# Optimization experiments

Hardware: AMD Instinct MI355X
Metric: run time of the kernel (lower is better)

## Reference

```python
import jax, jax.numpy as jnp
import numpy as np

BLOCK = 128
E, T, H, I, K = 16, 512, 2048, 1408, 6

def _dequant(w, s):
    # w: (E, R, C), s: (E, R//BLOCK, C//BLOCK) block-wise inverse scales
    return w * jnp.repeat(jnp.repeat(s, BLOCK, axis=1), BLOCK, axis=2)

def setup_inputs() -> dict:
    key = jax.random.key(0)
    ks = jax.random.split(key, 9)
    return {
        "x": jax.random.normal(ks[0], (T, H), dtype=jnp.float32),
        "gate_weights": jax.random.normal(ks[1], (E, I, H), dtype=jnp.float32) * 0.05,
        "gate_scales": jax.random.uniform(ks[2], (E, I // BLOCK, H // BLOCK), dtype=jnp.float32),
        "up_weights": jax.random.normal(ks[3], (E, I, H), dtype=jnp.float32) * 0.05,
        "up_scales": jax.random.uniform(ks[4], (E, I // BLOCK, H // BLOCK), dtype=jnp.float32),
        "down_weights": jax.random.normal(ks[5], (E, H, I), dtype=jnp.float32) * 0.05,
        "down_scales": jax.random.uniform(ks[6], (E, H // BLOCK, I // BLOCK), dtype=jnp.float32),
        "routing_weights": jax.random.uniform(ks[7], (T, K), dtype=jnp.float32),
        "selected_experts": jax.random.randint(ks[8], (T, K), 0, E, dtype=jnp.int32),
    }

def reference(x, gate_weights, gate_scales, up_weights, up_scales,
              down_weights, down_scales, routing_weights, selected_experts):
    # Dequantize block-quantized expert weights
    wg = _dequant(gate_weights, gate_scales)   # (E, I, H)
    wu = _dequant(up_weights, up_scales)       # (E, I, H)
    wd = _dequant(down_weights, down_scales)   # (E, H, I)
    # Dense per-expert grouped GEMMs (reference path: all experts see all tokens)
    g = jnp.einsum('th,eih->eti', x, wg)       # (E, T, I)
    u = jnp.einsum('th,eih->eti', x, wu)
    h = jax.nn.silu(g) * u                     # SwiGLU
    y = jnp.einsum('eti,ehi->eth', h, wd)      # (E, T, H)
    # Combine: top-k routing weights scattered to (T, E) then contracted
    onehot = jax.nn.one_hot(selected_experts, E, dtype=x.dtype)  # (T, K, E)
    combine = jnp.einsum('tk,tke->et', routing_weights, onehot)  # (E, T)
    return jnp.einsum('et,eth->th', combine, y)                  # (T, H)
```

## Files before the change

kernel.cpp:

```cpp
#include <hip/hip_runtime.h>
#include <stdint.h>

#define E_NUM 16
#define T_TOK 512
#define H_DIM 2048
#define I_DIM 1408
#define K_TOP 6
#define CAP   512

#define TM  256
#define TN  32
#define BK  64
#define LDA 72

typedef __attribute__((ext_vector_type(8))) __bf16 bf16x8;
typedef __attribute__((ext_vector_type(4))) float f32x4;
typedef __attribute__((ext_vector_type(4))) unsigned short us4;
typedef __attribute__((ext_vector_type(8))) unsigned short us8;

__device__ __forceinline__ unsigned short f2bf(float f) {
  union { float f; unsigned u; } v; v.f = f;
  unsigned r = v.u + 0x7FFFu + ((v.u >> 16) & 1u);
  return (unsigned short)(r >> 16);
}

__global__ void k_routing(const float* __restrict__ rw, const int* __restrict__ sel,
                          int* counts, int* list, float* cw) {
  int t = blockIdx.x * blockDim.x + threadIdx.x;
  if (t >= T_TOK) return;
  int e[K_TOP]; float w[K_TOP];
#pragma unroll
  for (int k = 0; k < K_TOP; ++k) { e[k] = sel[t*K_TOP+k]; w[k] = rw[t*K_TOP+k]; }
#pragma unroll
  for (int k = 0; k < K_TOP; ++k) {
    bool dup = false;
#pragma unroll
    for (int j = 0; j < K_TOP; ++j) if (j < k && e[j] == e[k]) dup = true;
    if (!dup) {
      float c = 0.f;
#pragma unroll
      for (int j = 0; j < K_TOP; ++j) if (e[j] == e[k]) c += w[j];
      int slot = atomicAdd(&counts[e[k]], 1);
      list[e[k]*CAP + slot] = t;
      cw[e[k]*CAP + slot] = c;
    }
  }
}

__global__ void k_xcast(const float* __restrict__ x, unsigned short* __restrict__ xb) {
  int i = blockIdx.x * blockDim.x + threadIdx.x;
  const float4* src = (const float4*)x;
  float4 v0 = src[2*i], v1 = src[2*i+1];
  us8 o;
  o[0]=f2bf(v0.x); o[1]=f2bf(v0.y); o[2]=f2bf(v0.z); o[3]=f2bf(v0.w);
  o[4]=f2bf(v1.x); o[5]=f2bf(v1.y); o[6]=f2bf(v1.z); o[7]=f2bf(v1.w);
  *(us8*)(xb + (size_t)i*8) = o;
}

__global__ __launch_bounds__(256, 2)
void k_gateup(const unsigned short* __restrict__ xb,
              const float* __restrict__ Wg, const float* __restrict__ Sg,
              const float* __restrict__ Wu, const float* __restrict__ Su,
              const int* __restrict__ counts, const int* __restrict__ list,
              const float* __restrict__ cw, unsigned short* __restrict__ Hbuf) {
  __shared__ unsigned short sA[TM * LDA];
  __shared__ unsigned short sB[2 * TN * LDA];
  const int e   = blockIdx.y;
  const int n0  = blockIdx.x * TN;
  const int cnt = counts[e];
  if (cnt == 0) return;
  const int tid  = threadIdx.x;
  const int wv   = tid >> 6;
  const int lane = tid & 63;
  const int quad = lane >> 4;
  const int ln   = lane & 15;

  const int*   listE = list + e * CAP;
  const float* cwE   = cw + e * CAP;
  const float* WgE = Wg + (size_t)e * I_DIM * H_DIM + (size_t)n0 * H_DIM;
  const float* WuE = Wu + (size_t)e * I_DIM * H_DIM + (size_t)n0 * H_DIM;
  const float* SgE = Sg + e * (11*16) + (n0 >> 7) * 16;
  const float* SuE = Su + e * (11*16) + (n0 >> 7) * 16;
  unsigned short* HbE = Hbuf + (size_t)e * CAP * I_DIM;

  for (int m0 = 0; m0 < cnt; m0 += TM) {
    int tok[8];
#pragma unroll
    for (int j = 0; j < 8; ++j) {
      int m = m0 + j*32 + (tid >> 3);
      tok[j] = (m < cnt) ? listE[m] : listE[0];
    }
    f32x4 accG[4][2], accU[4][2];
#pragma unroll
    for (int mi = 0; mi < 4; ++mi)
#pragma unroll
      for (int ni = 0; ni < 2; ++ni) {
        accG[mi][ni] = (f32x4){0.f,0.f,0.f,0.f};
        accU[mi][ni] = (f32x4){0.f,0.f,0.f,0.f};
      }

    for (int kc = 0; kc < H_DIM / BK; ++kc) {
      const int k0 = kc * BK;
      __syncthreads();
      const int seg = tid & 7;
#pragma unroll
      for (int j = 0; j < 8; ++j) {
        int row = j*32 + (tid >> 3);
        uint4 v = *(const uint4*)(xb + (size_t)tok[j]*H_DIM + k0 + seg*8);
        *(uint4*)(sA + row*LDA + seg*8) = v;
      }
      const float sG = SgE[k0 >> 7];
      const float sU = SuE[k0 >> 7];
#pragma unroll
      for (int j = 0; j < 4; ++j) {
        int p = j*256 + tid;
        int mat = p >> 9;
        int row = (p >> 4) & 31;
        int sg4 = p & 15;
        const float* W = (mat ? WuE : WgE) + (size_t)row * H_DIM + k0 + sg4*4;
        float s = mat ? sU : sG;
        float4 v = *(const float4*)W;
        us4 o;
        o.x = f2bf(v.x * s); o.y = f2bf(v.y * s);
        o.z = f2bf(v.z * s); o.w = f2bf(v.w * s);
        *(us4*)(sB + (mat*TN + row)*LDA + sg4*4) = o;
      }
      __syncthreads();
#pragma unroll
      for (int ks = 0; ks < 2; ++ks) {
        bf16x8 a[4], bg[2], bu[2];
#pragma unroll
        for (int mi = 0; mi < 4; ++mi)
          a[mi] = *(const bf16x8*)(sA + (wv*64 + mi*16 + ln)*LDA + ks*32 + quad*8);
#pragma unroll
        for (int ni = 0; ni < 2; ++ni) {
          bg[ni] = *(const bf16x8*)(sB + (ni*16 + ln)*LDA + ks*32 + quad*8);
          bu[ni] = *(const bf16x8*)(sB + (TN + ni*16 + ln)*LDA + ks*32 + quad*8);
        }
#pragma unroll
        for (int mi = 0; mi < 4; ++mi)
#pragma unroll
          for (int ni = 0; ni < 2; ++ni) {
            accG[mi][ni] = __builtin_amdgcn_mfma_f32_16x16x32_bf16(a[mi], bg[ni], accG[mi][ni], 0, 0, 0);
            accU[mi][ni] = __builtin_amdgcn_mfma_f32_16x16x32_bf16(a[mi], bu[ni], accU[mi][ni], 0, 0, 0);
          }
      }
    }
#pragma unroll
    for (int mi = 0; mi < 4; ++mi)
#pragma unroll
      for (int r = 0; r < 4; ++r) {
        int m = m0 + wv*64 + mi*16 + quad*4 + r;
        if (m < cnt) {
          float c = cwE[m];
#pragma unroll
          for (int ni = 0; ni < 2; ++ni) {
            float g = accG[mi][ni][r];
            float u = accU[mi][ni][r];
            float h = g / (1.f + __expf(-g)) * u * c;
            HbE[(size_t)m * I_DIM + n0 + ni*16 + ln] = f2bf(h);
          }
        }
      }
  }
}

__global__ __launch_bounds__(256, 2)
void k_down(const unsigned short* __restrict__ Hbuf,
            const float* __restrict__ Wd, const float* __restrict__ Sd,
            const int* __restrict__ counts, const int* __restrict__ list,
            float* __restrict__ out) {
  __shared__ unsigned short sA[TM * LDA];
  __shared__ unsigned short sB[TN * LDA];
  const int e   = blockIdx.y;
  const int n0  = blockIdx.x * TN;
  const int cnt = counts[e];
  if (cnt == 0) return;
  const int tid  = threadIdx.x;
  const int wv   = tid >> 6;
  const int lane = tid & 63;
  const int quad = lane >> 4;
  const int ln   = lane & 15;

  const int* listE = list + e * CAP;
  const unsigned short* HbE = Hbuf + (size_t)e * CAP * I_DIM;
  const float* WdE = Wd + (size_t)e * H_DIM * I_DIM + (size_t)n0 * I_DIM;
  const float* SdE = Sd + e * (16*11) + (n0 >> 7) * 11;

  for (int m0 = 0; m0 < cnt; m0 += TM) {
    f32x4 acc[4][2];
#pragma unroll
    for (int mi = 0; mi < 4; ++mi)
#pragma unroll
      for (int ni = 0; ni < 2; ++ni)
        acc[mi][ni] = (f32x4){0.f,0.f,0.f,0.f};

    for (int kc = 0; kc < I_DIM / BK; ++kc) {
      const int k0 = kc * BK;
      __syncthreads();
      const int seg = tid & 7;
#pragma unroll
      for (int j = 0; j < 8; ++j) {
        int row = j*32 + (tid >> 3);
        uint4 v = *(const uint4*)(HbE + (size_t)(m0 + row)*I_DIM + k0 + seg*8);
        *(uint4*)(sA + row*LDA + seg*8) = v;
      }
      const float s = SdE[k0 >> 7];
#pragma unroll
      for (int j = 0; j < 2; ++j) {
        int p = j*256 + tid;
        int row = p >> 4;
        int sg4 = p & 15;
        float4 v = *(const float4*)(WdE + (size_t)row * I_DIM + k0 + sg4*4);
        us4 o;
        o.x = f2bf(v.x * s); o.y = f2bf(v.y * s);
        o.z = f2bf(v.z * s); o.w = f2bf(v.w * s);
        *(us4*)(sB + row*LDA + sg4*4) = o;
      }
      __syncthreads();
#pragma unroll
      for (int ks = 0; ks < 2; ++ks) {
        bf16x8 a[4], b[2];
#pragma unroll
        for (int mi = 0; mi < 4; ++mi)
          a[mi] = *(const bf16x8*)(sA + (wv*64 + mi*16 + ln)*LDA + ks*32 + quad*8);
#pragma unroll
        for (int ni = 0; ni < 2; ++ni)
          b[ni] = *(const bf16x8*)(sB + (ni*16 + ln)*LDA + ks*32 + quad*8);
#pragma unroll
        for (int mi = 0; mi < 4; ++mi)
#pragma unroll
          for (int ni = 0; ni < 2; ++ni)
            acc[mi][ni] = __builtin_amdgcn_mfma_f32_16x16x32_bf16(a[mi], b[ni], acc[mi][ni], 0, 0, 0);
      }
    }
#pragma unroll
    for (int mi = 0; mi < 4; ++mi)
#pragma unroll
      for (int r = 0; r < 4; ++r) {
        int m = m0 + wv*64 + mi*16 + quad*4 + r;
        if (m < cnt) {
          int t = listE[m];
#pragma unroll
          for (int ni = 0; ni < 2; ++ni)
            atomicAdd(out + (size_t)t * H_DIM + n0 + ni*16 + ln, acc[mi][ni][r]);
        }
      }
  }
}

extern "C" void kernel_launch(void* const* d_in, const int* in_sizes, int n_in,
                              void* d_out, int out_size, void* d_ws, size_t ws_size,
                              hipStream_t stream) {
  const float* x  = (const float*)d_in[0];
  const float* Wg = (const float*)d_in[1];
  const float* Sg = (const float*)d_in[2];
  const float* Wu = (const float*)d_in[3];
  const float* Su = (const float*)d_in[4];
  const float* Wd = (const float*)d_in[5];
  const float* Sd = (const float*)d_in[6];
  const float* rw = (const float*)d_in[7];
  const int*  sel = (const int*)d_in[8];
  float* out = (float*)d_out;

  char* ws = (char*)d_ws;
  int*   counts = (int*)ws;
  int*   list   = (int*)(ws + 256);
  float* cw     = (float*)(ws + 256 + 32768);
  unsigned short* xb   = (unsigned short*)(ws + 256 + 65536);
  unsigned short* Hbuf = (unsigned short*)(ws + 256 + 65536 + (size_t)T_TOK*H_DIM*2);
  (void)in_sizes; (void)n_in; (void)out_size; (void)ws_size;

  hipMemsetAsync(counts, 0, 256, stream);
  hipMemsetAsync(out, 0, sizeof(float) * (size_t)T_TOK * H_DIM, stream);
  k_routing<<<dim3((T_TOK + 255) / 256), dim3(256), 0, stream>>>(rw, sel, counts, list, cw);
  k_xcast<<<dim3((T_TOK * H_DIM) / 2048), dim3(256), 0, stream>>>(x, xb);
  k_gateup<<<dim3(I_DIM / TN, E_NUM), dim3(256), 0, stream>>>(xb, Wg, Sg, Wu, Su, counts, list, cw, Hbuf);
  k_down<<<dim3(H_DIM / TN, E_NUM), dim3(256), 0, stream>>>(Hbuf, Wd, Sd, counts, list, out);
}
```

Measured before the change: 673.7 us.

## Drop LDS staging; load MFMA operands directly from global into registers

Both grouped GEMM kernels stop staging activations and dequantized weights through shared memory. Each wave now owns 16 (gate/up) or 32 (down) output columns and loads and dequantizes its weight fragment straight into MFMA operand registers. It also streams the token rows of activations directly from global/L2 for up to 256 tokens held in 16 register accumulators per matrix. This removes __syncthreads barriers and LDS traffic. The cost is uncoalesced 16-byte gathers of activation rows, much higher register pressure (32 f32x4 accumulators per thread), and a reshaped grid for the down kernel with expert-interleaved block indexing.

Result: slower. 848.3 us (+25.9%).

```diff
diff --git a/kernel.cpp b/kernel.cpp
--- a/kernel.cpp
+++ b/kernel.cpp
@@ -8,20 +8,21 @@
 #define K_TOP 6
 #define CAP   512
 
-#define TM  256
-#define TN  32
-#define BK  64
-#define LDA 72
-
 typedef __attribute__((ext_vector_type(8))) __bf16 bf16x8;
 typedef __attribute__((ext_vector_type(4))) float f32x4;
-typedef __attribute__((ext_vector_type(4))) unsigned short us4;
 typedef __attribute__((ext_vector_type(8))) unsigned short us8;
 
 __device__ __forceinline__ unsigned short f2bf(float f) {
   union { float f; unsigned u; } v; v.f = f;
   unsigned r = v.u + 0x7FFFu + ((v.u >> 16) & 1u);
   return (unsigned short)(r >> 16);
+}
+
+__device__ __forceinline__ bf16x8 pack8(float4 a, float4 b, float s) {
+  union { us8 u; bf16x8 h; } t;
+  t.u[0]=f2bf(a.x*s); t.u[1]=f2bf(a.y*s); t.u[2]=f2bf(a.z*s); t.u[3]=f2bf(a.w*s);
+  t.u[4]=f2bf(b.x*s); t.u[5]=f2bf(b.y*s); t.u[6]=f2bf(b.z*s); t.u[7]=f2bf(b.w*s);
+  return t.h;
 }
 
 __global__ void k_routing(const float* __restrict__ rw, const int* __restrict__ sel,
@@ -63,10 +64,7 @@
               const float* __restrict__ Wu, const float* __restrict__ Su,
               const int* __restrict__ counts, const int* __restrict__ list,
               const float* __restrict__ cw, unsigned short* __restrict__ Hbuf) {
-  __shared__ unsigned short sA[TM * LDA];
-  __shared__ unsigned short sB[2 * TN * LDA];
   const int e   = blockIdx.y;
-  const int n0  = blockIdx.x * TN;
   const int cnt = counts[e];
   if (cnt == 0) return;
   const int tid  = threadIdx.x;
@@ -74,94 +72,73 @@
   const int lane = tid & 63;
   const int quad = lane >> 4;
   const int ln   = lane & 15;
+  const int nb   = blockIdx.x * 64 + wv * 16;
 
   const int*   listE = list + e * CAP;
   const float* cwE   = cw + e * CAP;
-  const float* WgE = Wg + (size_t)e * I_DIM * H_DIM + (size_t)n0 * H_DIM;
-  const float* WuE = Wu + (size_t)e * I_DIM * H_DIM + (size_t)n0 * H_DIM;
-  const float* SgE = Sg + e * (11*16) + (n0 >> 7) * 16;
-  const float* SuE = Su + e * (11*16) + (n0 >> 7) * 16;
+  const float* wgRow = Wg + (size_t)e * I_DIM * H_DIM + (size_t)(nb + ln) * H_DIM;
+  const float* wuRow = Wu + (size_t)e * I_DIM * H_DIM + (size_t)(nb + ln) * H_DIM;
+  const float* SgE   = Sg + e * (11*16) + (nb >> 7) * 16;
+  const float* SuE   = Su + e * (11*16) + (nb >> 7) * 16;
   unsigned short* HbE = Hbuf + (size_t)e * CAP * I_DIM;
-
-  for (int m0 = 0; m0 < cnt; m0 += TM) {
-    int tok[8];
-#pragma unroll
-    for (int j = 0; j < 8; ++j) {
-      int m = m0 + j*32 + (tid >> 3);
-      tok[j] = (m < cnt) ? listE[m] : listE[0];
-    }
-    f32x4 accG[4][2], accU[4][2];
-#pragma unroll
-    for (int mi = 0; mi < 4; ++mi)
-#pragma unroll
-      for (int ni = 0; ni < 2; ++ni) {
-        accG[mi][ni] = (f32x4){0.f,0.f,0.f,0.f};
-        accU[mi][ni] = (f32x4){0.f,0.f,0.f,0.f};
-      }
-
-    for (int kc = 0; kc < H_DIM / BK; ++kc) {
-      const int k0 = kc * BK;
-      __syncthreads();
-      const int seg = tid & 7;
-#pragma unroll
-      for (int j = 0; j < 8; ++j) {
-        int row = j*32 + (tid >> 3);
-        uint4 v = *(const uint4*)(xb + (size_t)tok[j]*H_DIM + k0 + seg*8);
-        *(uint4*)(sA + row*LDA + seg*8) = v;
-      }
+  const char* xbB = (const char*)xb;
+
+  for (int m0 = 0; m0 < cnt; m0 += 256) {
+    const int rem   = cnt - m0;
+    const int miMax = (rem >= 256) ? 16 : ((rem + 15) >> 4);
+    unsigned tokoff[16];
+#pragma unroll
+    for (int mi = 0; mi < 16; ++mi) {
+      int m = m0 + mi*16 + ln;
+      tokoff[mi] = (unsigned)(listE[m < cnt ? m : 0] * (H_DIM * 2));
+    }
+    f32x4 accG[16], accU[16];
+#pragma unroll
+    for (int mi = 0; mi < 16; ++mi) {
+      accG[mi] = (f32x4){0.f,0.f,0.f,0.f};
+      accU[mi] = (f32x4){0.f,0.f,0.f,0.f};
+    }
+
+    for (int kc = 0; kc < H_DIM / 64; ++kc) {
+      const int k0 = kc * 64;
       const float sG = SgE[k0 >> 7];
       const float sU = SuE[k0 >> 7];
 #pragma unroll
-      for (int j = 0; j < 4; ++j) {
-        int p = j*256 + tid;
-        int mat = p >> 9;
-        int row = (p >> 4) & 31;
-        int sg4 = p & 15;
-        const float* W = (mat ? WuE : WgE) + (size_t)row * H_DIM + k0 + sg4*4;
-        float s = mat ? sU : sG;
-        float4 v = *(const float4*)W;
-        us4 o;
-        o.x = f2bf(v.x * s); o.y = f2bf(v.y * s);
-        o.z = f2bf(v.z * s); o.w = f2bf(v.w * s);
-        *(us4*)(sB + (mat*TN + row)*LDA + sg4*4) = o;
-      }
-      __syncthreads();
-#pragma unroll
       for (int ks = 0; ks < 2; ++ks) {
-        bf16x8 a[4], bg[2], bu[2];
-#pragma unroll
-        for (int mi = 0; mi < 4; ++mi)
-          a[mi] = *(const bf16x8*)(sA + (wv*64 + mi*16 + ln)*LDA + ks*32 + quad*8);
-#pragma unroll
-        for (int ni = 0; ni < 2; ++ni) {
-          bg[ni] = *(const bf16x8*)(sB + (ni*16 + ln)*LDA + ks*32 + quad*8);
-          bu[ni] = *(const bf16x8*)(sB + (TN + ni*16 + ln)*LDA + ks*32 + quad*8);
-        }
-#pragma unroll
-        for (int mi = 0; mi < 4; ++mi)
-#pragma unroll
-          for (int ni = 0; ni < 2; ++ni) {
-            accG[mi][ni] = __builtin_amdgcn_mfma_f32_16x16x32_bf16(a[mi], bg[ni], accG[mi][ni], 0, 0, 0);
-            accU[mi][ni] = __builtin_amdgcn_mfma_f32_16x16x32_bf16(a[mi], bu[ni], accU[mi][ni], 0, 0, 0);
-          }
-      }
-    }
-#pragma unroll
-    for (int mi = 0; mi < 4; ++mi)
-#pragma unroll
-      for (int r = 0; r < 4; ++r) {
-        int m = m0 + wv*64 + mi*16 + quad*4 + r;
-        if (m < cnt) {
-          float c = cwE[m];
-#pragma unroll
-          for (int ni = 0; ni < 2; ++ni) {
-            float g = accG[mi][ni][r];
-            float u = accU[mi][ni][r];
+        const int kk = k0 + ks*32 + quad*8;
+        float4 g0 = *(const float4*)(wgRow + kk);
+        float4 g1 = *(const float4*)(wgRow + kk + 4);
+        float4 u0 = *(const float4*)(wuRow + kk);
+        float4 u1 = *(const float4*)(wuRow + kk + 4);
+        bf16x8 bg = pack8(g0, g1, sG);
+        bf16x8 bu = pack8(u0, u1, sU);
+        const unsigned ko = (unsigned)(kk * 2);
+#pragma unroll
+        for (int mi = 0; mi < 16; ++mi) {
+          if (mi < miMax) {
+            bf16x8 a = *(const bf16x8*)(xbB + tokoff[mi] + ko);
+            accG[mi] = __builtin_amdgcn_mfma_f32_16x16x32_bf16(a, bg, accG[mi], 0, 0, 0);
+            accU[mi] = __builtin_amdgcn_mfma_f32_16x16x32_bf16(a, bu, accU[mi], 0, 0, 0);
+          }
+        }
+      }
+    }
+#pragma unroll
+    for (int mi = 0; mi < 16; ++mi) {
+      if (mi < miMax) {
+#pragma unroll
+        for (int r = 0; r < 4; ++r) {
+          int m = m0 + mi*16 + quad*4 + r;
+          if (m < cnt) {
+            float c = cwE[m];
+            float g = accG[mi][r];
+            float u = accU[mi][r];
             float h = g / (1.f + __expf(-g)) * u * c;
-            HbE[(size_t)m * I_DIM + n0 + ni*16 + ln] = f2bf(h);
-          }
-        }
-      }
+            HbE[(size_t)m * I_DIM + nb + ln] = f2bf(h);
+          }
+        }
+      }
+    }
   }
 }
 
@@ -170,82 +147,75 @@
             const float* __restrict__ Wd, const float* __restrict__ Sd,
             const int* __restrict__ counts, const int* __restrict__ list,
             float* __restrict__ out) {
-  __shared__ unsigned short sA[TM * LDA];
-  __shared__ unsigned short sB[TN * LDA];
-  const int e   = blockIdx.y;
-  const int n0  = blockIdx.x * TN;
-  const int cnt = counts[e];
+  const int bid  = blockIdx.x;
+  const int e    = bid & 15;
+  const int nblk = bid >> 4;
+  const int cnt  = counts[e];
   if (cnt == 0) return;
   const int tid  = threadIdx.x;
   const int wv   = tid >> 6;
   const int lane = tid & 63;
   const int quad = lane >> 4;
   const int ln   = lane & 15;
+  const int nb   = nblk * 128 + wv * 32;
 
   const int* listE = list + e * CAP;
-  const unsigned short* HbE = Hbuf + (size_t)e * CAP * I_DIM;
-  const float* WdE = Wd + (size_t)e * H_DIM * I_DIM + (size_t)n0 * I_DIM;
-  const float* SdE = Sd + e * (16*11) + (n0 >> 7) * 11;
-
-  for (int m0 = 0; m0 < cnt; m0 += TM) {
-    f32x4 acc[4][2];
-#pragma unroll
-    for (int mi = 0; mi < 4; ++mi)
-#pragma unroll
-      for (int ni = 0; ni < 2; ++ni)
-        acc[mi][ni] = (f32x4){0.f,0.f,0.f,0.f};
-
-    for (int kc = 0; kc < I_DIM / BK; ++kc) {
-      const int k0 = kc * BK;
-      __syncthreads();
-      const int seg = tid & 7;
-#pragma unroll
-      for (int j = 0; j < 8; ++j) {
-        int row = j*32 + (tid >> 3);
-        uint4 v = *(const uint4*)(HbE + (size_t)(m0 + row)*I_DIM + k0 + seg*8);
-        *(uint4*)(sA + row*LDA + seg*8) = v;
-      }
+  const char* HbB = (const char*)(Hbuf + (size_t)e * CAP * I_DIM);
+  const float* wd0 = Wd + (size_t)e * H_DIM * I_DIM + (size_t)(nb + ln) * I_DIM;
+  const float* wd1 = wd0 + (size_t)16 * I_DIM;
+  const float* SdE = Sd + e * (16*11) + (nb >> 7) * 11;
+
+  for (int m0 = 0; m0 < cnt; m0 += 256) {
+    const int rem   = cnt - m0;
+    const int miMax = (rem >= 256) ? 16 : ((rem + 15) >> 4);
+    unsigned rowoff[16];
+#pragma unroll
+    for (int mi = 0; mi < 16; ++mi)
+      rowoff[mi] = (unsigned)((m0 + mi*16 + ln) * (I_DIM * 2));
+    f32x4 acc0[16], acc1[16];
+#pragma unroll
+    for (int mi = 0; mi < 16; ++mi) {
+      acc0[mi] = (f32x4){0.f,0.f,0.f,0.f};
+      acc1[mi] = (f32x4){0.f,0.f,0.f,0.f};
+    }
+
+    for (int kc = 0; kc < I_DIM / 64; ++kc) {
+      const int k0 = kc * 64;
       const float s = SdE[k0 >> 7];
 #pragma unroll
-      for (int j = 0; j < 2; ++j) {
-        int p = j*256 + tid;
-        int row = p >> 4;
-        int sg4 = p & 15;
-        float4 v = *(const float4*)(WdE + (size_t)row * I_DIM + k0 + sg4*4);
-        us4 o;
-        o.x = f2bf(v.x * s); o.y = f2bf(v.y * s);
-        o.z = f2bf(v.z * s); o.w = f2bf(v.w * s);
-        *(us4*)(sB + row*LDA + sg4*4) = o;
-      }
-      __syncthreads();
-#pragma unroll
       for (int ks = 0; ks < 2; ++ks) {
-        bf16x8 a[4], b[2];
-#pragma unroll
-        for (int mi = 0; mi < 4; ++mi)
-          a[mi] = *(const bf16x8*)(sA + (wv*64 + mi*16 + ln)*LDA + ks*32 + quad*8);
-#pragma unroll
-        for (int ni = 0; ni < 2; ++ni)
-          b[ni] = *(const bf16x8*)(sB + (ni*16 + ln)*LDA + ks*32 + quad*8);
-#pragma unroll
-        for (int mi = 0; mi < 4; ++mi)
-#pragma unroll
-          for (int ni = 0; ni < 2; ++ni)
-            acc[mi][ni] = __builtin_amdgcn_mfma_f32_16x16x32_bf16(a[mi], b[ni], acc[mi][ni], 0, 0, 0);
-      }
-    }
-#pragma unroll
-    for (int mi = 0; mi < 4; ++mi)
-#pragma unroll
-      for (int r = 0; r < 4; ++r) {
-        int m = m0 + wv*64 + mi*16 + quad*4 + r;
-        if (m < cnt) {
-          int t = listE[m];
-#pragma unroll
-          for (int ni = 0; ni < 2; ++ni)
-            atomicAdd(out + (size_t)t * H_DIM + n0 + ni*16 + ln, acc[mi][ni][r]);
-        }
-      }
+        const int kk = k0 + ks*32 + quad*8;
+        float4 a0 = *(const float4*)(wd0 + kk);
+        float4 a1 = *(const float4*)(wd0 + kk + 4);
+        float4 c0 = *(const float4*)(wd1 + kk);
+        float4 c1 = *(const float4*)(wd1 + kk + 4);
+        bf16x8 b0 = pack8(a0, a1, s);
+        bf16x8 b1 = pack8(c0, c1, s);
+        const unsigned ko = (unsigned)(kk * 2);
+#pragma unroll
+        for (int mi = 0; mi < 16; ++mi) {
+          if (mi < miMax) {
+            bf16x8 a = *(const bf16x8*)(HbB + rowoff[mi] + ko);
+            acc0[mi] = __builtin_amdgcn_mfma_f32_16x16x32_bf16(a, b0, acc0[mi], 0, 0, 0);
+            acc1[mi] = __builtin_amdgcn_mfma_f32_16x16x32_bf16(a, b1, acc1[mi], 0, 0, 0);
+          }
+        }
+      }
+    }
+#pragma unroll
+    for (int mi = 0; mi < 16; ++mi) {
+      if (mi < miMax) {
+#pragma unroll
+        for (int r = 0; r < 4; ++r) {
+          int m = m0 + mi*16 + quad*4 + r;
+          if (m < cnt) {
+            int t = listE[m];
+            atomicAdd(out + (size_t)t * H_DIM + nb + ln,      acc0[mi][r]);
+            atomicAdd(out + (size_t)t * H_DIM + nb + 16 + ln, acc1[mi][r]);
+          }
+        }
+      }
+    }
   }
 }
 
@@ -275,6 +245,6 @@
   hipMemsetAsync(out, 0, sizeof(float) * (size_t)T_TOK * H_DIM, stream);
   k_routing<<<dim3((T_TOK + 255) / 256), dim3(256), 0, stream>>>(rw, sel, counts, list, cw);
   k_xcast<<<dim3((T_TOK * H_DIM) / 2048), dim3(256), 0, stream>>>(x, xb);
-  k_gateup<<<dim3(I_DIM / TN, E_NUM), dim3(256), 0, stream>>>(xb, Wg, Sg, Wu, Su, counts, list, cw, Hbuf);
-  k_down<<<dim3(H_DIM / TN, E_NUM), dim3(256), 0, stream>>>(Hbuf, Wd, Sd, counts, list, out);
-}
+  k_gateup<<<dim3(I_DIM / 64, E_NUM), dim3(256), 0, stream>>>(xb, Wg, Sg, Wu, Su, counts, list, cw, Hbuf);
+  k_down<<<dim3(256), dim3(256), 0, stream>>>(Hbuf, Wd, Sd, counts, list, out);
+}
```
